# Optimization experiments

Measured on AMD Instinct MI355X. Metric: run time of the kernel, lower is better.

The kernel has to match this reference:

```python
import jax, jax.numpy as jnp
import numpy as np
from jax.scipy.special import logsumexp

PAD_IDX, SOS_IDX, EOS_IDX = 0, 1, 2
NEG = -10000.0


def setup_inputs() -> dict:
    B, T, L = 64, 256, 8
    K, E, H = 128, 256, 512      # num_tags, EMBED_SIZE, HIDDEN_SIZE
    CV, WV = 128, 50000          # char / word vocab
    key = jax.random.key(0)
    ks = jax.random.split(key, 12)
    lengths = jax.random.randint(ks[0], (B,), T // 2, T + 1)
    mask = jnp.arange(T)[None, :] < lengths[:, None]          # [B,T] contiguous prefix
    wx = jnp.where(mask, jax.random.randint(ks[1], (B, T), 3, WV), 0).astype(jnp.int32)
    cx = jax.random.randint(ks[2], (B, T, L), 0, CV).astype(jnp.int32)
    y_body = jnp.where(mask, jax.random.randint(ks[3], (B, T), 3, K), PAD_IDX)
    y = jnp.concatenate([jnp.full((B, 1), SOS_IDX, jnp.int32), y_body.astype(jnp.int32)], 1)  # [B,T+1]
    s = 0.05
    char_emb = s * jax.random.normal(ks[4], (CV, E), jnp.float32)
    word_emb = s * jax.random.normal(ks[5], (WV, E), jnp.float32)
    Wi = s * jax.random.normal(ks[6], (E, 4 * H), jnp.float32)
    Wh = s * jax.random.normal(ks[7], (H, 4 * H), jnp.float32)
    b = jnp.zeros((4 * H,), jnp.float32)
    Wout = s * jax.random.normal(ks[8], (H, K), jnp.float32)
    bout = jnp.zeros((K,), jnp.float32)
    trans = jax.random.normal(ks[9], (K, K), jnp.float32)
    trans = trans.at[SOS_IDX, :].set(NEG)
    trans = trans.at[:, EOS_IDX].set(NEG)
    trans = trans.at[:, PAD_IDX].set(NEG)
    trans = trans.at[PAD_IDX, :].set(NEG)
    trans = trans.at[PAD_IDX, EOS_IDX].set(0.0)
    trans = trans.at[PAD_IDX, PAD_IDX].set(0.0)
    return dict(cx=cx, wx=wx, y=y, char_emb=char_emb, word_emb=word_emb,
                Wi=Wi, Wh=Wh, b=b, Wout=Wout, bout=bout, trans=trans)


def _forward(cx, wx, y, char_emb, word_emb, Wi, Wh, b, Wout, bout, trans):
    B, T = wx.shape
    K = trans.shape[0]
    H = Wh.shape[0]
    mask = (wx > 0)                                            # [B,T] bool
    maskf = mask.astype(jnp.float32)
    # embedding: word lookup + mean-pooled char lookup
    x = word_emb[wx] + char_emb[cx].mean(axis=2)               # [B,T,E]

    # masked LSTM (equivalent to pack_padded for prefix masks)
    def lstm_step(carry, inp):
        h, c = carry
        xt, mt = inp                                            # [B,E], [B,1]
        z = xt @ Wi + h @ Wh + b                                # [B,4H]
        i, f, g, o = jnp.split(z, 4, axis=-1)
        i, f, o = jax.nn.sigmoid(i), jax.nn.sigmoid(f), jax.nn.sigmoid(o)
        c_new = f * c + i * jnp.tanh(g)
        h_new = o * jnp.tanh(c_new)
        h = jnp.where(mt, h_new, h)
        c = jnp.where(mt, c_new, c)
        return (h, c), h

    h0 = jnp.zeros((B, H), x.dtype)
    xs = jnp.swapaxes(x, 0, 1)                                  # [T,B,E]
    ms = jnp.swapaxes(mask, 0, 1)[..., None]                    # [T,B,1]
    _, hs = jax.lax.scan(lstm_step, (h0, h0), (xs, ms))         # [T,B,H]
    hs = jnp.swapaxes(hs, 0, 1)                                 # [B,T,H]
    h = (hs @ Wout + bout) * maskf[..., None]                   # emissions [B,T,K]

    # CRF forward algorithm (log partition Z)
    score0 = jnp.full((B, K), NEG, h.dtype).at[:, SOS_IDX].set(0.0)

    def crf_step(score, inp):
        em, mt = inp                                            # [B,K], [B,1]
        s_t = logsumexp(score[:, None, :] + em[:, :, None] + trans[None, :, :], axis=-1)
        return jnp.where(mt, s_t, score), None

    emT = jnp.swapaxes(h, 0, 1)                                 # [T,B,K]
    scoreZ, _ = jax.lax.scan(crf_step, score0, (emT, ms))
    Z = logsumexp(scoreZ + trans[EOS_IDX], axis=-1)             # [B]

    # gold path score
    y_prev, y_next = y[:, :-1], y[:, 1:]                        # [B,T]
    emit = jnp.take_along_axis(h, y_next[..., None], axis=-1)[..., 0]  # [B,T]
    tr = trans[y_next, y_prev]                                  # [B,T]
    gold = jnp.sum((emit + tr) * maskf, axis=1)                 # [B]
    lengths = mask.sum(axis=1)
    last_tag = y[jnp.arange(B), lengths]                        # y has T+1 cols
    gold = gold + trans[EOS_IDX, last_tag]
    return Z - gold                                             # NLL per sequence [B]


def reference(cx, wx, y, char_emb, word_emb, Wi, Wh, b, Wout, bout, trans):
    return _forward(cx, wx, y, char_emb, word_emb, Wi, Wh, b, Wout, bout, trans)
```

## Files before the change

### kernel.cpp

```cpp
#include <hip/hip_runtime.h>


typedef float f32x4 __attribute__((ext_vector_type(4)));
typedef float f32x16 __attribute__((ext_vector_type(16)));
typedef __bf16 bf16x8 __attribute__((ext_vector_type(8)));
typedef unsigned int u32x4 __attribute__((ext_vector_type(4)));
typedef unsigned int u32x2 __attribute__((ext_vector_type(2)));

#define T_LEN 256
#define BB    64
#define EE    256
#define HH    512
#define KK    128
#define KCAT  768

static __device__ inline unsigned f2bf(float f) {
  union { float f; unsigned u; } v; v.f = f;
  unsigned r = v.u + 0x7FFF + ((v.u >> 16) & 1);
  return r >> 16;
}
static __device__ inline float sigm(float x) { return 1.f / (1.f + __expf(-x)); }
static __device__ inline float tanh_fast(float x) {
  return 1.f - 2.f / (1.f + __expf(2.f * x));
}
static __device__ inline bf16x8 ubf(u32x4 v) {
  union { u32x4 u; bf16x8 b; } c; c.u = v; return c.b;
}

__global__ __launch_bounds__(256) void build_wcat(
    const float* __restrict__ Wi, const float* __restrict__ Wh,
    unsigned short* __restrict__ WcatT) {
  __shared__ float tile[64][65];
  int ct = blockIdx.x & 31, kt = blockIdx.x >> 5;
  int tc = threadIdx.x & 63, tr = threadIdx.x >> 6;
  int c0 = ct * 64, k0 = kt * 64;
#pragma unroll
  for (int i = 0; i < 16; ++i) {
    int r = tr * 16 + i, k = k0 + r;
    float v = (k < EE) ? Wi[(size_t)k * 2048 + c0 + tc]
                       : Wh[(size_t)(k - EE) * 2048 + c0 + tc];
    tile[r][tc] = v;
  }
  __syncthreads();
#pragma unroll
  for (int i = 0; i < 16; ++i) {
    int cL = tr * 16 + i;
    WcatT[(size_t)(c0 + cL) * KCAT + k0 + tc] = (unsigned short)f2bf(tile[tc][cL]);
  }
}

__global__ __launch_bounds__(256) void build_wout(
    const float* __restrict__ Wout, unsigned short* __restrict__ WoutT) {
  __shared__ float tile[64][65];
  int ct = blockIdx.x & 1, kt = blockIdx.x >> 1;
  int tc = threadIdx.x & 63, tr = threadIdx.x >> 6;
  int c0 = ct * 64, k0 = kt * 64;
#pragma unroll
  for (int i = 0; i < 16; ++i) {
    int r = tr * 16 + i;
    tile[r][tc] = Wout[(size_t)(k0 + r) * KK + c0 + tc];
  }
  __syncthreads();
#pragma unroll
  for (int i = 0; i < 16; ++i) {
    int cL = tr * 16 + i;
    WoutT[(size_t)(c0 + cL) * HH + k0 + tc] = (unsigned short)f2bf(tile[tc][cL]);
  }
}

__global__ __launch_bounds__(256) void embed_kernel(
    const int* __restrict__ wx, const int* __restrict__ cx,
    const float* __restrict__ we, const float* __restrict__ ce,
    unsigned short* __restrict__ x) {
  int bid = blockIdx.x;
  int t = bid >> 6, b = bid & 63;
  int e = threadIdx.x;
  int w = wx[b * T_LEN + t];
  float v = we[(size_t)w * EE + e];
  const int* cp = cx + ((size_t)(b * T_LEN + t)) * 8;
  float s = 0.f;
#pragma unroll
  for (int l = 0; l < 8; ++l) s += ce[(size_t)cp[l] * EE + e];
  v += s * 0.125f;
  x[(size_t)bid * EE + e] = (unsigned short)f2bf(v);
}

__global__ void zero_flags(unsigned int* __restrict__ f) {
  unsigned z = 0u;
  asm volatile("global_store_dword %0, %1, off sc1"
               :: "v"(f + threadIdx.x), "v"(z) : "memory");
}

#define SBAR __builtin_amdgcn_sched_barrier(0)
#define WAITV(N) do { asm volatile("s_waitcnt vmcnt(" #N ")" ::: "memory"); SBAR; } while (0)
#define LDN(dst, ptr, OFF) \
  asm volatile("global_load_dwordx4 %0, %1, off offset:" OFF \
               : "=v"(dst) : "v"(ptr) : "memory")

#define ISSUE_X(B, P) do { \
  LDN(B[0],P,"0");   LDN(B[1],P,"32");  LDN(B[2],P,"64");  LDN(B[3],P,"96"); \
  LDN(B[4],P,"128"); LDN(B[5],P,"160"); LDN(B[6],P,"192"); LDN(B[7],P,"224"); \
  LDN(B[8],P,"256"); LDN(B[9],P,"288"); LDN(B[10],P,"320"); LDN(B[11],P,"352"); \
  LDN(B[12],P,"384"); LDN(B[13],P,"416"); LDN(B[14],P,"448"); LDN(B[15],P,"480"); } while (0)
#define ISSUE_H0(B, P) do { \
  LDN(B[0],P,"0");   LDN(B[1],P,"32");  LDN(B[2],P,"64");  LDN(B[3],P,"96"); \
  LDN(B[4],P,"128"); LDN(B[5],P,"160"); LDN(B[6],P,"192"); LDN(B[7],P,"224"); \
  LDN(B[8],P,"256"); LDN(B[9],P,"288"); LDN(B[10],P,"320"); LDN(B[11],P,"352"); \
  LDN(B[12],P,"384"); LDN(B[13],P,"416"); LDN(B[14],P,"448"); LDN(B[15],P,"480"); } while (0)
#define ISSUE_H1(B, P) do { \
  LDN(B[0],P,"512"); LDN(B[1],P,"544"); LDN(B[2],P,"576"); LDN(B[3],P,"608"); \
  LDN(B[4],P,"640"); LDN(B[5],P,"672"); LDN(B[6],P,"704"); LDN(B[7],P,"736"); \
  LDN(B[8],P,"768"); LDN(B[9],P,"800"); LDN(B[10],P,"832"); LDN(B[11],P,"864"); \
  LDN(B[12],P,"896"); LDN(B[13],P,"928"); LDN(B[14],P,"960"); LDN(B[15],P,"992"); } while (0)

#define GATES_STORE(T) do { \
    bool mk = ((int)wxv) > 0; \
    _Pragma("unroll") \
    for (int r = 0; r < 4; ++r) { \
      float zi = acc[r], zf = acc[4 + r], zg = acc[8 + r], zo = acc[12 + r]; \
      float cn = sigm(zf) * cst[r] + sigm(zi) * tanh_fast(zg); \
      float hn = sigm(zo) * tanh_fast(cn); \
      if (mk) { cst[r] = cn; hst[r] = hn; } \
    } \
    u32x2 ph; \
    ph[0] = f2bf(hst[0]) | (f2bf(hst[1]) << 16); \
    ph[1] = f2bf(hst[2]) | (f2bf(hst[3]) << 16); \
    asm volatile("global_store_dwordx2 %0, %1, off sc1" \
                 :: "v"(hstore + (size_t)(T) * 65536), "v"(ph) : "memory"); \
  } while (0)

__global__ __launch_bounds__(128, 1) void lstm_persistent(
    const unsigned short* __restrict__ x,
    unsigned short* __restrict__ hs,
    const unsigned short* __restrict__ WcatT,
    const float* __restrict__ bias,
    const int* __restrict__ wx,
    unsigned int* __restrict__ flags) {
  const int tid = threadIdx.x;
  const int lane = tid & 63;
  const int bhalf = tid >> 6;
  const int hi = lane >> 5;
  const int batch = bhalf * 32 + (lane & 31);
  const int u0 = blockIdx.x * 8;
  const int rr = lane & 31;
  const int wcol = (rr >> 3) * HH + u0 + (rr & 7);

  bf16x8 wreg[48];
#pragma unroll
  for (int kf = 0; kf < 48; ++kf)
    wreg[kf] = *(const bf16x8*)(WcatT + (size_t)wcol * KCAT + kf * 16 + hi * 8);

  float bv[16];
#pragma unroll
  for (int q = 0; q < 4; ++q)
#pragma unroll
    for (int r = 0; r < 4; ++r)
      bv[q * 4 + r] = bias[q * HH + u0 + 4 * hi + r];

  const char* xlane  = (const char*)x  + ((size_t)batch * EE + hi * 8) * 2;
  const char* hread  = (const char*)hs + ((size_t)batch * HH + hi * 8) * 2;
  char*       hstore = (char*)hs + ((size_t)batch * HH + u0 + 4 * hi) * 2;
  const int*  wxp    = wx + batch * T_LEN;

  float cst[4] = {0.f, 0.f, 0.f, 0.f};
  float hst[4] = {0.f, 0.f, 0.f, 0.f};
  u32x4 bufX[16], bufH[16];
  unsigned wxv;
  f32x16 acc;

  ISSUE_X(bufX, xlane);
  asm volatile("global_load_dword %0, %1, off" : "=v"(wxv) : "v"(wxp) : "memory");
  WAITV(0);
#pragma unroll
  for (int i = 0; i < 16; ++i) acc[i] = bv[i];
#pragma unroll
  for (int kf = 0; kf < 16; ++kf)
    acc = __builtin_amdgcn_mfma_f32_32x32x16_bf16(wreg[kf], ubf(bufX[kf]), acc, 0, 0, 0);
  GATES_STORE(0);
  WAITV(0);
  __syncthreads();
  if (tid == 0)
    __hip_atomic_store(flags + blockIdx.x, 1u, __ATOMIC_RELAXED, __HIP_MEMORY_SCOPE_AGENT);

  for (int t = 1; t < T_LEN; ++t) {
    const char* xt = xlane + (size_t)t * 32768;
    const char* hp = hread + (size_t)(t - 1) * 65536;

    ISSUE_X(bufX, xt);
    asm volatile("global_load_dword %0, %1, off" : "=v"(wxv) : "v"(wxp + t) : "memory");
    {
      unsigned v;
      do {
        asm volatile("global_load_dword %0, %1, off sc1\n\ts_waitcnt vmcnt(0)"
                     : "=v"(v) : "v"(flags + lane) : "memory");
      } while (!__all((int)(v >= (unsigned)t)));
      SBAR;
    }
    ISSUE_H0(bufH, hp);
#pragma unroll
    for (int i = 0; i < 16; ++i) acc[i] = bv[i];
#pragma unroll
    for (int kf = 0; kf < 16; ++kf)
      acc = __builtin_amdgcn_mfma_f32_32x32x16_bf16(wreg[kf], ubf(bufX[kf]), acc, 0, 0, 0);
    SBAR;
    ISSUE_H1(bufX, hp);
    WAITV(16);
#pragma unroll
    for (int kf = 0; kf < 16; ++kf)
      acc = __builtin_amdgcn_mfma_f32_32x32x16_bf16(wreg[16 + kf], ubf(bufH[kf]), acc, 0, 0, 0);
    WAITV(0);
#pragma unroll
    for (int kf = 0; kf < 16; ++kf)
      acc = __builtin_amdgcn_mfma_f32_32x32x16_bf16(wreg[32 + kf], ubf(bufX[kf]), acc, 0, 0, 0);
    GATES_STORE(t);
    WAITV(0);
    __syncthreads();
    if (tid == 0)
      __hip_atomic_store(flags + blockIdx.x, (unsigned)(t + 1),
                         __ATOMIC_RELAXED, __HIP_MEMORY_SCOPE_AGENT);
  }
}

__global__ __launch_bounds__(512) void em_gemm(
    const unsigned short* __restrict__ hs,
    const unsigned short* __restrict__ WoutT,
    const float* __restrict__ bout,
    const int* __restrict__ wx,
    float* __restrict__ em) {
  int mg = blockIdx.x;
  int wave = threadIdx.x >> 6, lane = threadIdx.x & 63;
  int m = wave >> 1, nh = wave & 1;
  int arow = lane & 15, kg = (lane >> 4) * 8;
  int rbase = mg * 64 + m * 16;
  const unsigned short* A = hs + (size_t)(rbase + arow) * HH + kg;
  f32x4 acc[4];
#pragma unroll
  for (int nt = 0; nt < 4; ++nt) acc[nt] = (f32x4){0.f, 0.f, 0.f, 0.f};
#pragma unroll
  for (int ks = 0; ks < 16; ++ks) {
    bf16x8 a = *(const bf16x8*)(A + ks * 32);
#pragma unroll
    for (int nt = 0; nt < 4; ++nt) {
      const unsigned short* Bp =
          WoutT + (size_t)(nh * 64 + nt * 16 + arow) * HH + kg + ks * 32;
      acc[nt] = __builtin_amdgcn_mfma_f32_16x16x32_bf16(a, *(const bf16x8*)Bp, acc[nt], 0, 0, 0);
    }
  }
#pragma unroll
  for (int nt = 0; nt < 4; ++nt) {
    int n = nh * 64 + nt * 16 + arow;
    float bo = bout[n];
#pragma unroll
    for (int r = 0; r < 4; ++r) {
      int row = rbase + (lane >> 4) * 4 + r;
      int t = row >> 6, b = row & 63;
      float v = (acc[nt][r] + bo) * ((wx[b * T_LEN + t] > 0) ? 1.f : 0.f);
      em[(size_t)row * KK + n] = v;
    }
  }
}

__global__ __launch_bounds__(512) void crf_kernel(
    const float* __restrict__ em,
    const float* __restrict__ trans,
    const int* __restrict__ wx,
    const int* __restrict__ y,
    float* __restrict__ out) {
  int b = blockIdx.x;
  __shared__ float tl[KK][129];
  __shared__ float El[KK][129];
  __shared__ float sc[KK];
  __shared__ float p[KK];
  __shared__ float red[512];
  __shared__ float red2[512];
  __shared__ float mshare[2];
  int tid = threadIdx.x;
  for (int i = tid; i < KK * KK; i += 512) {
    float v = trans[i];
    tl[i >> 7][i & 127] = v;
    El[i >> 7][i & 127] = __expf(v);
  }
  if (tid < KK) sc[tid] = (tid == 1) ? 0.f : -10000.f;
  __syncthreads();

  int k = tid & 127, q = tid >> 7, j0 = q * 32;
  float msc = 0.f;

  for (int t = 0; t < T_LEN; ++t) {
    if (wx[b * T_LEN + t] <= 0) continue;
    if (tid < KK) p[tid] = __expf(sc[tid] - msc);
    __syncthreads();
    float S = 0.f;
#pragma unroll
    for (int j = 0; j < 32; ++j) S += El[k][j0 + j] * p[j0 + j];
    red[tid] = S;
    __syncthreads();
    if (q == 0) {
      float Sk = S + red[128 + k] + red[256 + k] + red[384 + k];
      float ns = em[(size_t)(t * BB + b) * KK + k] + msc + __logf(Sk);
      sc[k] = ns;
      float m = ns;
#pragma unroll
      for (int off = 32; off; off >>= 1) m = fmaxf(m, __shfl_xor(m, off));
      if ((tid & 63) == 0) mshare[tid >> 6] = m;
    }
    __syncthreads();
    msc = fmaxf(mshare[0], mshare[1]);
  }

  float term = 0.f, cnt = 0.f;
  if (tid < T_LEN) {
    int yp = y[b * 257 + tid], yn = y[b * 257 + tid + 1];
    if (wx[b * T_LEN + tid] > 0) {
      term = em[(size_t)(tid * BB + b) * KK + yn] + tl[yn][yp];
      cnt = 1.f;
    }
  }
  red[tid] = term; red2[tid] = cnt;
  __syncthreads();
  for (int s2 = 256; s2 > 0; s2 >>= 1) {
    if (tid < s2) { red[tid] += red[tid + s2]; red2[tid] += red2[tid + s2]; }
    __syncthreads();
  }
  float gold = red[0];
  int len = (int)(red2[0] + 0.5f);
  __syncthreads();

  float v = (tid < KK) ? sc[tid] + tl[2][tid] : -3.0e38f;
  red[tid] = v;
  __syncthreads();
  for (int s2 = 256; s2 > 0; s2 >>= 1) {
    if (tid < s2) red[tid] = fmaxf(red[tid], red[tid + s2]);
    __syncthreads();
  }
  float mz = red[0];
  __syncthreads();
  red[tid] = (tid < KK) ? __expf(v - mz) : 0.f;
  __syncthreads();
  for (int s2 = 256; s2 > 0; s2 >>= 1) {
    if (tid < s2) red[tid] += red[tid + s2];
    __syncthreads();
  }
  if (tid == 0) {
    float Z = mz + __logf(red[0]);
    int last_tag = y[b * 257 + len];
    out[b] = Z - (gold + tl[2][last_tag]);
  }
}

extern "C" void kernel_launch(void* const* d_in, const int* in_sizes, int n_in,
                              void* d_out, int out_size, void* d_ws, size_t ws_size,
                              hipStream_t stream) {
  const int*   cx    = (const int*)d_in[0];
  const int*   wx    = (const int*)d_in[1];
  const int*   y     = (const int*)d_in[2];
  const float* ce    = (const float*)d_in[3];
  const float* we    = (const float*)d_in[4];
  const float* Wi    = (const float*)d_in[5];
  const float* Wh    = (const float*)d_in[6];
  const float* bias  = (const float*)d_in[7];
  const float* Wout  = (const float*)d_in[8];
  const float* bout  = (const float*)d_in[9];
  const float* trans = (const float*)d_in[10];
  float* out = (float*)d_out;

  char* ws = (char*)d_ws;
  unsigned short* WcatT = (unsigned short*)(ws + 0);
  unsigned short* WoutT = (unsigned short*)(ws + 3145728);
  unsigned short* x     = (unsigned short*)(ws + 3276800);
  unsigned short* hs    = (unsigned short*)(ws + 11665408);
  unsigned int*   flags = (unsigned int*)(ws + 28442624);
  float*          em    = (float*)(ws + 3276800);

  build_wcat<<<384, 256, 0, stream>>>(Wi, Wh, WcatT);
  build_wout<<<16, 256, 0, stream>>>(Wout, WoutT);
  embed_kernel<<<T_LEN * BB, 256, 0, stream>>>(wx, cx, we, ce, x);
  zero_flags<<<1, 64, 0, stream>>>(flags);
  lstm_persistent<<<64, 128, 0, stream>>>(x, hs, WcatT, bias, wx, flags);
  em_gemm<<<256, 512, 0, stream>>>(hs, WoutT, bout, wx, em);
  crf_kernel<<<BB, 512, 0, stream>>>(em, trans, wx, y, out);
}
```

Measured before the change: 1.616 ms.

## Fuse LSTM, emission GEMM and CRF into one persistent flag-pipelined kernel

Replaces the separate LSTM, emission GEMM and CRF launches with a single persistent kernel of 136 blocks. 64 blocks run the LSTM, 8 blocks compute per-timestep emissions as soon as the LSTM flags show h_t is ready, and 64 blocks run the CRF forward recursion, polling per-timestep emission flags. The aim is to hide the GEMM and the serial CRF recursion behind the LSTM critical path and to remove launch gaps. The CRF reductions also move to wave shuffles with 128 threads per batch item. In exchange it relies on all 136 blocks being co-resident, and it adds spin polling with an iteration cap that could read stale data if the cap is hit.

```diff
diff --git a/kernel.cpp b/kernel.cpp
--- a/kernel.cpp
+++ b/kernel.cpp
@@ -86,9 +86,12 @@
 }
 
 __global__ void zero_flags(unsigned int* __restrict__ f) {
-  unsigned z = 0u;
-  asm volatile("global_store_dword %0, %1, off sc1"
-               :: "v"(f + threadIdx.x), "v"(z) : "memory");
+  int i = threadIdx.x;
+  if (i < 320) {
+    unsigned z = 0u;
+    asm volatile("global_store_dword %0, %1, off sc1"
+                 :: "v"(f + i), "v"(z) : "memory");
+  }
 }
 
 #define SBAR __builtin_amdgcn_sched_barrier(0)
@@ -98,11 +101,6 @@
                : "=v"(dst) : "v"(ptr) : "memory")
 
 #define ISSUE_X(B, P) do { \
-  LDN(B[0],P,"0");   LDN(B[1],P,"32");  LDN(B[2],P,"64");  LDN(B[3],P,"96"); \
-  LDN(B[4],P,"128"); LDN(B[5],P,"160"); LDN(B[6],P,"192"); LDN(B[7],P,"224"); \
-  LDN(B[8],P,"256"); LDN(B[9],P,"288"); LDN(B[10],P,"320"); LDN(B[11],P,"352"); \
-  LDN(B[12],P,"384"); LDN(B[13],P,"416"); LDN(B[14],P,"448"); LDN(B[15],P,"480"); } while (0)
-#define ISSUE_H0(B, P) do { \
   LDN(B[0],P,"0");   LDN(B[1],P,"32");  LDN(B[2],P,"64");  LDN(B[3],P,"96"); \
   LDN(B[4],P,"128"); LDN(B[5],P,"160"); LDN(B[6],P,"192"); LDN(B[7],P,"224"); \
   LDN(B[8],P,"256"); LDN(B[9],P,"288"); LDN(B[10],P,"320"); LDN(B[11],P,"352"); \
@@ -129,222 +127,238 @@
                  :: "v"(hstore + (size_t)(T) * 65536), "v"(ph) : "memory"); \
   } while (0)
 
-__global__ __launch_bounds__(128, 1) void lstm_persistent(
+__global__ __launch_bounds__(128, 1) void fused_kernel(
     const unsigned short* __restrict__ x,
     unsigned short* __restrict__ hs,
     const unsigned short* __restrict__ WcatT,
+    const unsigned short* __restrict__ WoutT,
     const float* __restrict__ bias,
-    const int* __restrict__ wx,
-    unsigned int* __restrict__ flags) {
-  const int tid = threadIdx.x;
-  const int lane = tid & 63;
-  const int bhalf = tid >> 6;
-  const int hi = lane >> 5;
-  const int batch = bhalf * 32 + (lane & 31);
-  const int u0 = blockIdx.x * 8;
-  const int rr = lane & 31;
-  const int wcol = (rr >> 3) * HH + u0 + (rr & 7);
-
-  bf16x8 wreg[48];
-#pragma unroll
-  for (int kf = 0; kf < 48; ++kf)
-    wreg[kf] = *(const bf16x8*)(WcatT + (size_t)wcol * KCAT + kf * 16 + hi * 8);
-
-  float bv[16];
-#pragma unroll
-  for (int q = 0; q < 4; ++q)
-#pragma unroll
-    for (int r = 0; r < 4; ++r)
-      bv[q * 4 + r] = bias[q * HH + u0 + 4 * hi + r];
-
-  const char* xlane  = (const char*)x  + ((size_t)batch * EE + hi * 8) * 2;
-  const char* hread  = (const char*)hs + ((size_t)batch * HH + hi * 8) * 2;
-  char*       hstore = (char*)hs + ((size_t)batch * HH + u0 + 4 * hi) * 2;
-  const int*  wxp    = wx + batch * T_LEN;
-
-  float cst[4] = {0.f, 0.f, 0.f, 0.f};
-  float hst[4] = {0.f, 0.f, 0.f, 0.f};
-  u32x4 bufX[16], bufH[16];
-  unsigned wxv;
-  f32x16 acc;
-
-  ISSUE_X(bufX, xlane);
-  asm volatile("global_load_dword %0, %1, off" : "=v"(wxv) : "v"(wxp) : "memory");
-  WAITV(0);
-#pragma unroll
-  for (int i = 0; i < 16; ++i) acc[i] = bv[i];
-#pragma unroll
-  for (int kf = 0; kf < 16; ++kf)
-    acc = __builtin_amdgcn_mfma_f32_32x32x16_bf16(wreg[kf], ubf(bufX[kf]), acc, 0, 0, 0);
-  GATES_STORE(0);
-  WAITV(0);
-  __syncthreads();
-  if (tid == 0)
-    __hip_atomic_store(flags + blockIdx.x, 1u, __ATOMIC_RELAXED, __HIP_MEMORY_SCOPE_AGENT);
-
-  for (int t = 1; t < T_LEN; ++t) {
-    const char* xt = xlane + (size_t)t * 32768;
-    const char* hp = hread + (size_t)(t - 1) * 65536;
-
-    ISSUE_X(bufX, xt);
-    asm volatile("global_load_dword %0, %1, off" : "=v"(wxv) : "v"(wxp + t) : "memory");
-    {
-      unsigned v;
-      do {
-        asm volatile("global_load_dword %0, %1, off sc1\n\ts_waitcnt vmcnt(0)"
-                     : "=v"(v) : "v"(flags + lane) : "memory");
-      } while (!__all((int)(v >= (unsigned)t)));
-      SBAR;
-    }
-    ISSUE_H0(bufH, hp);
-#pragma unroll
-    for (int i = 0; i < 16; ++i) acc[i] = bv[i];
-#pragma unroll
-    for (int kf = 0; kf < 16; ++kf)
-      acc = __builtin_amdgcn_mfma_f32_32x32x16_bf16(wreg[kf], ubf(bufX[kf]), acc, 0, 0, 0);
-    SBAR;
-    ISSUE_H1(bufX, hp);
-    WAITV(16);
-#pragma unroll
-    for (int kf = 0; kf < 16; ++kf)
-      acc = __builtin_amdgcn_mfma_f32_32x32x16_bf16(wreg[16 + kf], ubf(bufH[kf]), acc, 0, 0, 0);
-    WAITV(0);
-#pragma unroll
-    for (int kf = 0; kf < 16; ++kf)
-      acc = __builtin_amdgcn_mfma_f32_32x32x16_bf16(wreg[32 + kf], ubf(bufX[kf]), acc, 0, 0, 0);
-    GATES_STORE(t);
-    WAITV(0);
-    __syncthreads();
-    if (tid == 0)
-      __hip_atomic_store(flags + blockIdx.x, (unsigned)(t + 1),
-                         __ATOMIC_RELAXED, __HIP_MEMORY_SCOPE_AGENT);
-  }
-}
-
-__global__ __launch_bounds__(512) void em_gemm(
-    const unsigned short* __restrict__ hs,
-    const unsigned short* __restrict__ WoutT,
     const float* __restrict__ bout,
-    const int* __restrict__ wx,
-    float* __restrict__ em) {
-  int mg = blockIdx.x;
-  int wave = threadIdx.x >> 6, lane = threadIdx.x & 63;
-  int m = wave >> 1, nh = wave & 1;
-  int arow = lane & 15, kg = (lane >> 4) * 8;
-  int rbase = mg * 64 + m * 16;
-  const unsigned short* A = hs + (size_t)(rbase + arow) * HH + kg;
-  f32x4 acc[4];
-#pragma unroll
-  for (int nt = 0; nt < 4; ++nt) acc[nt] = (f32x4){0.f, 0.f, 0.f, 0.f};
-#pragma unroll
-  for (int ks = 0; ks < 16; ++ks) {
-    bf16x8 a = *(const bf16x8*)(A + ks * 32);
-#pragma unroll
-    for (int nt = 0; nt < 4; ++nt) {
-      const unsigned short* Bp =
-          WoutT + (size_t)(nh * 64 + nt * 16 + arow) * HH + kg + ks * 32;
-      acc[nt] = __builtin_amdgcn_mfma_f32_16x16x32_bf16(a, *(const bf16x8*)Bp, acc[nt], 0, 0, 0);
-    }
-  }
-#pragma unroll
-  for (int nt = 0; nt < 4; ++nt) {
-    int n = nh * 64 + nt * 16 + arow;
-    float bo = bout[n];
-#pragma unroll
-    for (int r = 0; r < 4; ++r) {
-      int row = rbase + (lane >> 4) * 4 + r;
-      int t = row >> 6, b = row & 63;
-      float v = (acc[nt][r] + bo) * ((wx[b * T_LEN + t] > 0) ? 1.f : 0.f);
-      em[(size_t)row * KK + n] = v;
-    }
-  }
-}
-
-__global__ __launch_bounds__(512) void crf_kernel(
-    const float* __restrict__ em,
     const float* __restrict__ trans,
     const int* __restrict__ wx,
     const int* __restrict__ y,
+    float* __restrict__ em,
+    unsigned int* __restrict__ flags,
+    unsigned int* __restrict__ emflag,
     float* __restrict__ out) {
-  int b = blockIdx.x;
-  __shared__ float tl[KK][129];
-  __shared__ float El[KK][129];
-  __shared__ float sc[KK];
-  __shared__ float p[KK];
-  __shared__ float red[512];
-  __shared__ float red2[512];
-  __shared__ float mshare[2];
-  int tid = threadIdx.x;
-  for (int i = tid; i < KK * KK; i += 512) {
-    float v = trans[i];
-    tl[i >> 7][i & 127] = v;
-    El[i >> 7][i & 127] = __expf(v);
-  }
-  if (tid < KK) sc[tid] = (tid == 1) ? 0.f : -10000.f;
-  __syncthreads();
-
-  int k = tid & 127, q = tid >> 7, j0 = q * 32;
-  float msc = 0.f;
-
-  for (int t = 0; t < T_LEN; ++t) {
-    if (wx[b * T_LEN + t] <= 0) continue;
-    if (tid < KK) p[tid] = __expf(sc[tid] - msc);
-    __syncthreads();
-    float S = 0.f;
-#pragma unroll
-    for (int j = 0; j < 32; ++j) S += El[k][j0 + j] * p[j0 + j];
-    red[tid] = S;
-    __syncthreads();
-    if (q == 0) {
-      float Sk = S + red[128 + k] + red[256 + k] + red[384 + k];
-      float ns = em[(size_t)(t * BB + b) * KK + k] + msc + __logf(Sk);
-      sc[k] = ns;
+  __shared__ float s_tl[KK][129];
+  __shared__ float s_El[KK][129];
+  __shared__ float s_p[KK];
+  __shared__ float s_red[16];
+
+  const int bid = blockIdx.x;
+  const int tid = threadIdx.x;
+  const int wave = tid >> 6, lane = tid & 63;
+
+  if (bid < 64) {
+    const int bhalf = wave;
+    const int hi = lane >> 5;
+    const int batch = bhalf * 32 + (lane & 31);
+    const int u0 = bid * 8;
+    const int rr = lane & 31;
+    const int wcol = (rr >> 3) * HH + u0 + (rr & 7);
+
+    bf16x8 wreg[48];
+#pragma unroll
+    for (int kf = 0; kf < 48; ++kf)
+      wreg[kf] = *(const bf16x8*)(WcatT + (size_t)wcol * KCAT + kf * 16 + hi * 8);
+
+    float bv[16];
+#pragma unroll
+    for (int q = 0; q < 4; ++q)
+#pragma unroll
+      for (int r = 0; r < 4; ++r)
+        bv[q * 4 + r] = bias[q * HH + u0 + 4 * hi + r];
+
+    const char* xlane  = (const char*)x  + ((size_t)batch * EE + hi * 8) * 2;
+    const char* hread  = (const char*)hs + ((size_t)batch * HH + hi * 8) * 2;
+    char*       hstore = (char*)hs + ((size_t)batch * HH + u0 + 4 * hi) * 2;
+    const int*  wxp    = wx + batch * T_LEN;
+
+    float cst[4] = {0.f, 0.f, 0.f, 0.f};
+    float hst[4] = {0.f, 0.f, 0.f, 0.f};
+    u32x4 bufX[16], bufH[16];
+    unsigned wxv;
+    f32x16 acc;
+
+    ISSUE_X(bufX, xlane);
+    asm volatile("global_load_dword %0, %1, off" : "=v"(wxv) : "v"(wxp) : "memory");
+    WAITV(0);
+#pragma unroll
+    for (int i = 0; i < 16; ++i) acc[i] = bv[i];
+#pragma unroll
+    for (int kf = 0; kf < 16; ++kf)
+      acc = __builtin_amdgcn_mfma_f32_32x32x16_bf16(wreg[kf], ubf(bufX[kf]), acc, 0, 0, 0);
+    GATES_STORE(0);
+    WAITV(0);
+    __syncthreads();
+    if (tid == 0)
+      __hip_atomic_store(flags + bid, 1u, __ATOMIC_RELAXED, __HIP_MEMORY_SCOPE_AGENT);
+
+    for (int t = 1; t < T_LEN; ++t) {
+      const char* xt = xlane + (size_t)t * 32768;
+      const char* hp = hread + (size_t)(t - 1) * 65536;
+
+      ISSUE_X(bufX, xt);
+      asm volatile("global_load_dword %0, %1, off" : "=v"(wxv) : "v"(wxp + t) : "memory");
+      {
+        unsigned v;
+        do {
+          asm volatile("global_load_dword %0, %1, off sc1\n\ts_waitcnt vmcnt(0)"
+                       : "=v"(v) : "v"(flags + lane) : "memory");
+        } while (!__all((int)(v >= (unsigned)t)));
+        SBAR;
+      }
+      ISSUE_X(bufH, hp);
+#pragma unroll
+      for (int i = 0; i < 16; ++i) acc[i] = bv[i];
+#pragma unroll
+      for (int kf = 0; kf < 16; ++kf)
+        acc = __builtin_amdgcn_mfma_f32_32x32x16_bf16(wreg[kf], ubf(bufX[kf]), acc, 0, 0, 0);
+      SBAR;
+      ISSUE_H1(bufX, hp);
+      WAITV(16);
+#pragma unroll
+      for (int kf = 0; kf < 16; ++kf)
+        acc = __builtin_amdgcn_mfma_f32_32x32x16_bf16(wreg[16 + kf], ubf(bufH[kf]), acc, 0, 0, 0);
+      WAITV(0);
+#pragma unroll
+      for (int kf = 0; kf < 16; ++kf)
+        acc = __builtin_amdgcn_mfma_f32_32x32x16_bf16(wreg[32 + kf], ubf(bufX[kf]), acc, 0, 0, 0);
+      GATES_STORE(t);
+      WAITV(0);
+      __syncthreads();
+      if (tid == 0)
+        __hip_atomic_store(flags + bid, (unsigned)(t + 1),
+                           __ATOMIC_RELAXED, __HIP_MEMORY_SCOPE_AGENT);
+    }
+  } else if (bid < 72) {
+    const int et0 = bid - 64;
+    const int arow = lane & 15, kg4 = (lane >> 4) * 8;
+    for (int i = 0; i < 32; ++i) {
+      const int t = et0 + 8 * i;
+      {
+        unsigned v; int it = 0;
+        for (;;) {
+          asm volatile("global_load_dword %0, %1, off sc1\n\ts_waitcnt vmcnt(0)"
+                       : "=v"(v) : "v"(flags + lane) : "memory");
+          if (__all((int)(v >= (unsigned)(t + 1)))) break;
+          if (++it >= (1 << 17)) break;
+        }
+        SBAR;
+      }
+      const unsigned short* A0 = hs + ((size_t)t * BB + wave * 32 + arow) * HH + kg4;
+      f32x4 acc2[2][8];
+#pragma unroll
+      for (int mt = 0; mt < 2; ++mt)
+#pragma unroll
+        for (int nt = 0; nt < 8; ++nt) acc2[mt][nt] = (f32x4){0.f, 0.f, 0.f, 0.f};
+#pragma unroll
+      for (int ks = 0; ks < 16; ++ks) {
+        bf16x8 a0 = *(const bf16x8*)(A0 + ks * 32);
+        bf16x8 a1 = *(const bf16x8*)(A0 + 16 * HH + ks * 32);
+#pragma unroll
+        for (int nt = 0; nt < 8; ++nt) {
+          bf16x8 bf = *(const bf16x8*)(WoutT + (size_t)(nt * 16 + arow) * HH + kg4 + ks * 32);
+          acc2[0][nt] = __builtin_amdgcn_mfma_f32_16x16x32_bf16(a0, bf, acc2[0][nt], 0, 0, 0);
+          acc2[1][nt] = __builtin_amdgcn_mfma_f32_16x16x32_bf16(a1, bf, acc2[1][nt], 0, 0, 0);
+        }
+      }
+#pragma unroll
+      for (int nt = 0; nt < 8; ++nt) {
+        int n = nt * 16 + arow;
+        float bo = bout[n];
+#pragma unroll
+        for (int mt = 0; mt < 2; ++mt)
+#pragma unroll
+          for (int r = 0; r < 4; ++r) {
+            int row = t * BB + wave * 32 + mt * 16 + (lane >> 4) * 4 + r;
+            float val = acc2[mt][nt][r] + bo;
+            asm volatile("global_store_dword %0, %1, off sc1"
+                         :: "v"(em + (size_t)row * KK + n), "v"(val) : "memory");
+          }
+      }
+      WAITV(0);
+      __syncthreads();
+      if (tid == 0)
+        __hip_atomic_store(emflag + t, 1u, __ATOMIC_RELAXED, __HIP_MEMORY_SCOPE_AGENT);
+    }
+  } else {
+    const int b = bid - 72;
+    const int k = tid;
+    for (int i2 = tid; i2 < KK * KK; i2 += 128) {
+      float v = trans[i2];
+      s_tl[i2 >> 7][i2 & 127] = v;
+      s_El[i2 >> 7][i2 & 127] = __expf(v);
+    }
+    __syncthreads();
+    float sck = (k == 1) ? 0.f : -10000.f;
+    float msc = 0.f;
+
+    for (int t = 0; t < T_LEN; ++t) {
+      if (wx[b * T_LEN + t] <= 0) continue;
+      {
+        unsigned v; int it = 0;
+        for (;;) {
+          asm volatile("global_load_dword %0, %1, off sc1\n\ts_waitcnt vmcnt(0)"
+                       : "=v"(v) : "v"(emflag + t) : "memory");
+          if (v) break;
+          if (++it >= (1 << 17)) break;
+        }
+        SBAR;
+      }
+      s_p[k] = __expf(sck - msc);
+      __syncthreads();
+      float S = 0.f;
+#pragma unroll
+      for (int j = 0; j < KK; ++j) S += s_El[k][j] * s_p[j];
+      float ns = em[((size_t)t * BB + b) * KK + k] + msc + __logf(S);
+      sck = ns;
       float m = ns;
 #pragma unroll
       for (int off = 32; off; off >>= 1) m = fmaxf(m, __shfl_xor(m, off));
-      if ((tid & 63) == 0) mshare[tid >> 6] = m;
-    }
-    __syncthreads();
-    msc = fmaxf(mshare[0], mshare[1]);
-  }
-
-  float term = 0.f, cnt = 0.f;
-  if (tid < T_LEN) {
-    int yp = y[b * 257 + tid], yn = y[b * 257 + tid + 1];
-    if (wx[b * T_LEN + tid] > 0) {
-      term = em[(size_t)(tid * BB + b) * KK + yn] + tl[yn][yp];
-      cnt = 1.f;
-    }
-  }
-  red[tid] = term; red2[tid] = cnt;
-  __syncthreads();
-  for (int s2 = 256; s2 > 0; s2 >>= 1) {
-    if (tid < s2) { red[tid] += red[tid + s2]; red2[tid] += red2[tid + s2]; }
-    __syncthreads();
-  }
-  float gold = red[0];
-  int len = (int)(red2[0] + 0.5f);
-  __syncthreads();
-
-  float v = (tid < KK) ? sc[tid] + tl[2][tid] : -3.0e38f;
-  red[tid] = v;
-  __syncthreads();
-  for (int s2 = 256; s2 > 0; s2 >>= 1) {
-    if (tid < s2) red[tid] = fmaxf(red[tid], red[tid + s2]);
-    __syncthreads();
-  }
-  float mz = red[0];
-  __syncthreads();
-  red[tid] = (tid < KK) ? __expf(v - mz) : 0.f;
-  __syncthreads();
-  for (int s2 = 256; s2 > 0; s2 >>= 1) {
-    if (tid < s2) red[tid] += red[tid + s2];
-    __syncthreads();
-  }
-  if (tid == 0) {
-    float Z = mz + __logf(red[0]);
-    int last_tag = y[b * 257 + len];
-    out[b] = Z - (gold + tl[2][last_tag]);
+      if (lane == 0) s_red[8 + wave] = m;
+      __syncthreads();
+      msc = fmaxf(s_red[8], s_red[9]);
+    }
+
+    float term = 0.f, cnt = 0.f;
+#pragma unroll
+    for (int rep = 0; rep < 2; ++rep) {
+      int tt = tid + rep * 128;
+      int yp = y[b * 257 + tt], yn = y[b * 257 + tt + 1];
+      if (wx[b * T_LEN + tt] > 0) {
+        term += em[((size_t)tt * BB + b) * KK + yn] + s_tl[yn][yp];
+        cnt += 1.f;
+      }
+    }
+#pragma unroll
+    for (int off = 32; off; off >>= 1) {
+      term += __shfl_xor(term, off);
+      cnt += __shfl_xor(cnt, off);
+    }
+    if (lane == 0) { s_red[wave] = term; s_red[2 + wave] = cnt; }
+    __syncthreads();
+    float gold = s_red[0] + s_red[1];
+    int len = (int)(s_red[2] + s_red[3] + 0.5f);
+
+    float v = sck + s_tl[2][k];
+    float mz = v;
+#pragma unroll
+    for (int off = 32; off; off >>= 1) mz = fmaxf(mz, __shfl_xor(mz, off));
+    if (lane == 0) s_red[4 + wave] = mz;
+    __syncthreads();
+    mz = fmaxf(s_red[4], s_red[5]);
+    float e = __expf(v - mz);
+#pragma unroll
+    for (int off = 32; off; off >>= 1) e += __shfl_xor(e, off);
+    if (lane == 0) s_red[6 + wave] = e;
+    __syncthreads();
+    if (tid == 0) {
+      float Z = mz + __logf(s_red[6] + s_red[7]);
+      int last_tag = y[b * 257 + len];
+      out[b] = Z - (gold + s_tl[2][last_tag]);
+    }
   }
 }
 
@@ -370,13 +384,13 @@
   unsigned short* x     = (unsigned short*)(ws + 3276800);
   unsigned short* hs    = (unsigned short*)(ws + 11665408);
   unsigned int*   flags = (unsigned int*)(ws + 28442624);
-  float*          em    = (float*)(ws + 3276800);
+  unsigned int*   emflag= (unsigned int*)(ws + 28442880);
+  float*          em    = (float*)(ws + 28444672);
 
   build_wcat<<<384, 256, 0, stream>>>(Wi, Wh, WcatT);
   build_wout<<<16, 256, 0, stream>>>(Wout, WoutT);
   embed_kernel<<<T_LEN * BB, 256, 0, stream>>>(wx, cx, we, ce, x);
-  zero_flags<<<1, 64, 0, stream>>>(flags);
-  lstm_persistent<<<64, 128, 0, stream>>>(x, hs, WcatT, bias, wx, flags);
-  em_gemm<<<256, 512, 0, stream>>>(hs, WoutT, bout, wx, em);
-  crf_kernel<<<BB, 512, 0, stream>>>(em, trans, wx, y, out);
-}
+  zero_flags<<<1, 320, 0, stream>>>(flags);
+  fused_kernel<<<136, 128, 0, stream>>>(x, hs, WcatT, WoutT, bias, bout, trans,
+                                        wx, y, em, flags, emflag, out);
+}
```

Measured after the change: 1.463 ms. 9.5% less time.
